# Optimization experiments

Measured on AMD Instinct MI355X. Metric: run time of the kernel, lower is better.

The kernel has to match this reference:

```python
import jax, jax.numpy as jnp
import numpy as np

N_NODES = 100000
N_EDGES = 1600000
D_IN = 32
D_OUT = 32
K_HOPS = 2
CUTGRAPH = 0.2
EPS = 1e-12  # torch F.normalize eps


def setup_inputs() -> dict:
    key = jax.random.key(0)
    k1, k2, k3, k4 = jax.random.split(key, 4)
    features = jax.random.normal(k1, (N_NODES, D_IN), dtype=jnp.float32)
    W = jax.random.normal(k2, (D_OUT, D_IN), dtype=jnp.float32) * (1.0 / np.sqrt(D_IN))
    src = jax.random.randint(k3, (N_EDGES,), 0, N_NODES, dtype=jnp.int64 if jax.config.jax_enable_x64 else jnp.int32)
    dst = jax.random.randint(k4, (N_EDGES,), 0, N_NODES, dtype=jnp.int64 if jax.config.jax_enable_x64 else jnp.int32)
    return {"features": features, "W": W, "src": src, "dst": dst}


def reference(features, W, src, dst):
    N = features.shape[0]
    E = src.shape[0]
    cut_k = int(E * CUTGRAPH)  # static edge count to prune

    # symmetric degree norm: deg^{-1/2} over in-degrees, clamped at 1
    deg = jax.ops.segment_sum(jnp.ones((E,), features.dtype), dst, num_segments=N)
    norm = jnp.power(jnp.clip(deg, 1.0, None), -0.5)[:, None]  # [N,1]

    h = features
    for _ in range(K_HOPS):
        # cosine-similarity edge pruning: zero the cut_k lowest-cos edges
        nrm = jnp.linalg.norm(h, axis=-1, keepdims=True)
        nh = h / jnp.maximum(nrm, EPS)  # F.normalize(p=2)
        cos = jnp.sum(nh[src] * nh[dst], axis=-1)  # [E]
        _, low_idx = jax.lax.top_k(-cos, cut_k)    # indices of smallest cos
        w = jnp.ones((E,), h.dtype).at[low_idx].set(0.0)

        h = h * norm
        msg = h[src] * w[:, None]                       # u_mul_e gather [E,D]
        h = jax.ops.segment_sum(msg, dst, num_segments=N)  # sum scatter
        h = h * norm

    return h @ W.T  # fc (bias=False)
```

## Files before the change

kernel.cpp:

```cpp
#include <hip/hip_runtime.h>
#include <hip/hip_bf16.h>
#include <stdint.h>

#define N_NODES 100000
#define N_EDGES 1600000
#define D_FEAT 32
#define CUT_K 320000
#define COSKEY_NB 4096
#define HC_NB 1000
#define HC_SLICE 1600
#define SCAN_NB ((N_NODES + 255) / 256)

struct SelState { unsigned long long prefix; unsigned int k; };

__global__ void deg_kernel(const int* __restrict__ dst, int* __restrict__ deg, int E) {
    int e = blockIdx.x * blockDim.x + threadIdx.x;
    if (e < E) atomicAdd(&deg[dst[e]], 1);
}

__global__ void norm_kernel(const int* __restrict__ deg, float* __restrict__ nrm, int N) {
    int i = blockIdx.x * blockDim.x + threadIdx.x;
    if (i < N) nrm[i] = 1.0f / sqrtf(fmaxf((float)deg[i], 1.0f));
}

__global__ void blocksum_kernel(const int* __restrict__ deg, int* __restrict__ bsum, int N) {
    int i = blockIdx.x * 256 + threadIdx.x;
    int v = (i < N) ? deg[i] : 0;
#pragma unroll
    for (int off = 32; off > 0; off >>= 1) v += __shfl_down(v, off, 64);
    __shared__ int ws4[4];
    if ((threadIdx.x & 63) == 0) ws4[threadIdx.x >> 6] = v;
    __syncthreads();
    if (threadIdx.x == 0) bsum[blockIdx.x] = ws4[0] + ws4[1] + ws4[2] + ws4[3];
}

__global__ void scanpartial_kernel(const int* __restrict__ bsum, int* __restrict__ boff, int B) {
    __shared__ int buf[512];
    int t = threadIdx.x;
    int v = (t < B) ? bsum[t] : 0;
    buf[t] = v;
    __syncthreads();
    for (int off = 1; off < 512; off <<= 1) {
        int u = (t >= off) ? buf[t - off] : 0;
        __syncthreads();
        buf[t] += u;
        __syncthreads();
    }
    if (t < B) boff[t] = buf[t] - v;
}

__global__ void writeoffs_kernel(const int* __restrict__ deg, const int* __restrict__ boff,
                                 int* __restrict__ offs, int* __restrict__ cursor, int N) {
    __shared__ int buf[256];
    int t = threadIdx.x;
    int i = blockIdx.x * 256 + t;
    int v = (i < N) ? deg[i] : 0;
    buf[t] = v;
    __syncthreads();
    for (int off = 1; off < 256; off <<= 1) {
        int u = (t >= off) ? buf[t - off] : 0;
        __syncthreads();
        buf[t] += u;
        __syncthreads();
    }
    int ex = buf[t] - v + boff[blockIdx.x];
    if (i < N) { offs[i] = ex; cursor[i] = ex; }
    if (i == N - 1) offs[N] = ex + v;
}

__global__ void fill_kernel(const int* __restrict__ src, const int* __restrict__ dst,
                            int* __restrict__ cursor,
                            int* __restrict__ csr_src, int* __restrict__ csr_dst,
                            int* __restrict__ csr_eid, int E) {
    int e = blockIdx.x * blockDim.x + threadIdx.x;
    if (e >= E) return;
    int d = dst[e];
    int pos = atomicAdd(&cursor[d], 1);
    csr_src[pos] = src[e];
    csr_dst[pos] = d;
    csr_eid[pos] = e;
}

__global__ void rownorm_kernel(const float* __restrict__ h, float* __restrict__ nh,
                               float* __restrict__ hs, const float* __restrict__ nrm,
                               SelState* __restrict__ st, int N) {
    int i = blockIdx.x * blockDim.x + threadIdx.x;
    if (i == 0) { st->prefix = 0ull; st->k = CUT_K; }
    if (i >= N) return;
    const float4* hp = (const float4*)(h + (size_t)i * D_FEAT);
    float4 v[8];
    float ss = 0.f;
#pragma unroll
    for (int q = 0; q < 8; ++q) {
        v[q] = hp[q];
        ss += v[q].x * v[q].x + v[q].y * v[q].y + v[q].z * v[q].z + v[q].w * v[q].w;
    }
    float inv = 1.0f / fmaxf(sqrtf(ss), 1e-12f);
    float sc = nrm[i];
    float4* op = (float4*)(nh + (size_t)i * D_FEAT);
    float4* sp = (float4*)(hs + (size_t)i * D_FEAT);
#pragma unroll
    for (int q = 0; q < 8; ++q) {
        float4 ov = v[q];
        float4 sv = v[q];
        ov.x *= inv; ov.y *= inv; ov.z *= inv; ov.w *= inv;
        sv.x *= sc;  sv.y *= sc;  sv.z *= sc;  sv.w *= sc;
        op[q] = ov;
        sp[q] = sv;
    }
}

__global__ void coskey_kernel(const float* __restrict__ nh, const int* __restrict__ csr_src,
                              const int* __restrict__ csr_dst, const int* __restrict__ csr_eid,
                              unsigned long long* __restrict__ keys,
                              unsigned int* __restrict__ ghist, int E) {
    __shared__ unsigned int lh[4][256];
    int t = threadIdx.x;
#pragma unroll
    for (int w = 0; w < 4; ++w) lh[w][t] = 0u;
    __syncthreads();
    int wave = t >> 6;
    int stride = gridDim.x * blockDim.x;
    for (int p = blockIdx.x * blockDim.x + t; p < E; p += stride) {
        const float4* a = (const float4*)(nh + (size_t)csr_src[p] * D_FEAT);
        const float4* b = (const float4*)(nh + (size_t)csr_dst[p] * D_FEAT);
        float s = 0.f;
#pragma unroll
        for (int q = 0; q < 8; ++q) {
            float4 x = a[q], y = b[q];
            s += x.x * y.x + x.y * y.y + x.z * y.z + x.w * y.w;
        }
        unsigned int u = __float_as_uint(s);
        unsigned int so = (u & 0x80000000u) ? ~u : (u | 0x80000000u);
        unsigned long long key = ((unsigned long long)so << 32) | (unsigned int)csr_eid[p];
        keys[p] = key;
        atomicAdd(&lh[wave][(unsigned int)(key >> 56)], 1u);
    }
    __syncthreads();
    unsigned int tot = lh[0][t] + lh[1][t] + lh[2][t] + lh[3][t];
    if (tot) atomicAdd(&ghist[t], tot);
}

__global__ void histc_kernel(const unsigned long long* __restrict__ in,
                             const int* __restrict__ cnt_in,
                             unsigned long long* __restrict__ out,
                             int* __restrict__ cnt_out,
                             const SelState* __restrict__ st,
                             unsigned int* __restrict__ ghist, int pass) {
    __shared__ unsigned int lh[4][256];
    __shared__ unsigned int lcnt;
    int t = threadIdx.x, b = blockIdx.x;
#pragma unroll
    for (int w = 0; w < 4; ++w) lh[w][t] = 0u;
    if (t == 0) lcnt = 0u;
    __syncthreads();
    unsigned long long prefix = st->prefix;
    int n = cnt_in ? cnt_in[b] : HC_SLICE;
    const unsigned long long* sin = in + (size_t)b * HC_SLICE;
    unsigned long long* sout = out + (size_t)b * HC_SLICE;
    int wave = t >> 6;
    int fshift = 64 - 8 * pass;
    int dshift = 56 - 8 * pass;
    for (int i = t; i < n; i += 256) {
        unsigned long long key = sin[i];
        if ((key >> fshift) == prefix) {
            atomicAdd(&lh[wave][(unsigned int)((key >> dshift) & 0xFFull)], 1u);
            unsigned int slot = atomicAdd(&lcnt, 1u);
            sout[slot] = key;
        }
    }
    __syncthreads();
    if (t == 0) cnt_out[b] = (int)lcnt;
    unsigned int tot = lh[0][t] + lh[1][t] + lh[2][t] + lh[3][t];
    if (tot) atomicAdd(&ghist[t], tot);
}

__global__ void scan8_kernel(unsigned int* __restrict__ ghist, SelState* __restrict__ st) {
    __shared__ unsigned int buf[256];
    int t = threadIdx.x;
    unsigned int k = st->k;
    unsigned int s = ghist[t];
    buf[t] = s;
    __syncthreads();
    for (int off = 1; off < 256; off <<= 1) {
        unsigned int v = (t >= off) ? buf[t - off] : 0u;
        __syncthreads();
        buf[t] += v;
        __syncthreads();
    }
    unsigned int incl = buf[t];
    unsigned int excl = incl - s;
    if (excl < k && k <= incl) {
        st->prefix = (st->prefix << 8) | (unsigned long long)t;
        st->k = k - excl;
    }
    ghist[t] = 0u;
}

__global__ void aggregate_csr_kernel(const float* __restrict__ hs, float* __restrict__ h_out,
                                     const int* __restrict__ offs, const int* __restrict__ csr_src,
                                     const unsigned long long* __restrict__ keys,
                                     const SelState* __restrict__ st,
                                     const float* __restrict__ nrm, int N) {
    unsigned long long kth = st->prefix;
    int g = blockIdx.x * 8 + (threadIdx.x >> 5);
    int j = threadIdx.x & 31;
    if (g >= N) return;
    int lo = offs[g], hi = offs[g + 1];
    float acc = 0.f;
    int p = lo;
    for (; p + 8 <= hi; p += 8) {
        unsigned long long kk[8];
        int ss[8];
#pragma unroll
        for (int u = 0; u < 8; ++u) { kk[u] = keys[p + u]; ss[u] = csr_src[p + u]; }
        float vv[8];
#pragma unroll
        for (int u = 0; u < 8; ++u) vv[u] = hs[(size_t)ss[u] * D_FEAT + j];
#pragma unroll
        for (int u = 0; u < 8; ++u) acc += (kk[u] > kth) ? vv[u] : 0.f;
    }
    for (; p < hi; ++p) {
        if (keys[p] > kth) acc += hs[(size_t)csr_src[p] * D_FEAT + j];
    }
    h_out[(size_t)g * D_FEAT + j] = acc * nrm[g];
}

__global__ void fc_kernel(const float* __restrict__ h, const float* __restrict__ W,
                          float* __restrict__ out, int N) {
    __shared__ float Wt[32][33];
    int t = threadIdx.x;
    for (int i = t; i < 1024; i += 256) Wt[i & 31][i >> 5] = W[i];
    __syncthreads();
    int node = blockIdx.x * 8 + (t >> 5);
    if (node >= N) return;
    int o = t & 31;
    const float* hr = h + (size_t)node * D_FEAT;
    float acc = 0.f;
#pragma unroll
    for (int j = 0; j < 32; ++j) acc += hr[j] * Wt[j][o];
    out[(size_t)node * D_FEAT + o] = acc;
}

extern "C" void kernel_launch(void* const* d_in, const int* in_sizes, int n_in,
                              void* d_out, int out_size, void* d_ws, size_t ws_size,
                              hipStream_t stream) {
    const float* features = (const float*)d_in[0];
    const float* W        = (const float*)d_in[1];
    const int*   src      = (const int*)d_in[2];
    const int*   dst      = (const int*)d_in[3];
    float*       out      = (float*)d_out;

    char* ws = (char*)d_ws;
    size_t o = 0;
    auto take = [&](size_t bytes) -> char* {
        char* p = ws + o;
        o += (bytes + 255) & ~(size_t)255;
        return p;
    };
    int*                deg     = (int*)take((size_t)N_NODES * 4);
    float*              nrm     = (float*)take((size_t)N_NODES * 4);
    int*                offs    = (int*)take((size_t)(N_NODES + 1) * 4);
    int*                cursor  = (int*)take((size_t)N_NODES * 4);
    int*                csr_src = (int*)take((size_t)N_EDGES * 4);
    int*                csr_dst = (int*)take((size_t)N_EDGES * 4);
    int*                csr_eid = (int*)take((size_t)N_EDGES * 4);
    float*              hA      = (float*)take((size_t)N_NODES * D_FEAT * 4);
    float*              hB      = (float*)take((size_t)N_NODES * D_FEAT * 4);
    float*              nh      = (float*)take((size_t)N_NODES * D_FEAT * 4);
    float*              hs      = (float*)take((size_t)N_NODES * D_FEAT * 4);
    unsigned long long* keys    = (unsigned long long*)take((size_t)N_EDGES * 8);
    unsigned int*       ghist   = (unsigned int*)take((size_t)256 * 4);
    SelState*           st      = (SelState*)take(256);
    int*                bsum    = (int*)take((size_t)SCAN_NB * 4);
    int*                boff    = (int*)take((size_t)SCAN_NB * 4);
    int*                cnt_a   = (int*)take((size_t)HC_NB * 4);
    int*                cnt_b   = (int*)take((size_t)HC_NB * 4);

    unsigned long long* candA = (unsigned long long*)nh;
    unsigned long long* candB = (unsigned long long*)hB;

    hipMemsetAsync(deg, 0, (size_t)N_NODES * 4, stream);
    hipMemsetAsync(ghist, 0, (size_t)256 * 4, stream);

    deg_kernel<<<(N_EDGES + 255) / 256, 256, 0, stream>>>(dst, deg, N_EDGES);
    norm_kernel<<<(N_NODES + 255) / 256, 256, 0, stream>>>(deg, nrm, N_NODES);
    blocksum_kernel<<<SCAN_NB, 256, 0, stream>>>(deg, bsum, N_NODES);
    scanpartial_kernel<<<1, 512, 0, stream>>>(bsum, boff, SCAN_NB);
    writeoffs_kernel<<<SCAN_NB, 256, 0, stream>>>(deg, boff, offs, cursor, N_NODES);
    fill_kernel<<<(N_EDGES + 255) / 256, 256, 0, stream>>>(src, dst, cursor,
                                                           csr_src, csr_dst, csr_eid, N_EDGES);

    const float* hin = features;
    float* houts[2] = { hA, hB };
    for (int hop = 0; hop < 2; ++hop) {
        float* hout = houts[hop];
        rownorm_kernel<<<(N_NODES + 255) / 256, 256, 0, stream>>>(hin, nh, hs, nrm, st, N_NODES);
        coskey_kernel<<<COSKEY_NB, 256, 0, stream>>>(nh, csr_src, csr_dst, csr_eid,
                                                     keys, ghist, N_EDGES);
        scan8_kernel<<<1, 256, 0, stream>>>(ghist, st);
        for (int pass = 1; pass < 8; ++pass) {
            const unsigned long long* in =
                (pass == 1) ? keys : ((pass & 1) ? candB : candA);
            const int* cin = (pass == 1) ? (const int*)nullptr
                                         : ((pass & 1) ? cnt_b : cnt_a);
            unsigned long long* outc = (pass & 1) ? candA : candB;
            int* cout = (pass & 1) ? cnt_a : cnt_b;
            histc_kernel<<<HC_NB, 256, 0, stream>>>(in, cin, outc, cout, st, ghist, pass);
            scan8_kernel<<<1, 256, 0, stream>>>(ghist, st);
        }
        aggregate_csr_kernel<<<(N_NODES + 7) / 8, 256, 0, stream>>>(
            hs, hout, offs, csr_src, keys, st, nrm, N_NODES);
        hin = hout;
    }
    fc_kernel<<<(N_NODES + 7) / 8, 256, 0, stream>>>(hin, W, out, N_NODES);
}
```

Before: 634.4 us.

## Collapse radix-select passes 2-7 into one single-block finish kernel; drop csr_dst

```diff
diff --git a/kernel.cpp b/kernel.cpp
--- a/kernel.cpp
+++ b/kernel.cpp
@@ -68,16 +68,11 @@
     if (i == N - 1) offs[N] = ex + v;
 }
 
-__global__ void fill_kernel(const int* __restrict__ src, const int* __restrict__ dst,
-                            int* __restrict__ cursor,
-                            int* __restrict__ csr_src, int* __restrict__ csr_dst,
+__global__ void fill_kernel(const int* __restrict__ dst, int* __restrict__ cursor,
                             int* __restrict__ csr_eid, int E) {
     int e = blockIdx.x * blockDim.x + threadIdx.x;
     if (e >= E) return;
-    int d = dst[e];
-    int pos = atomicAdd(&cursor[d], 1);
-    csr_src[pos] = src[e];
-    csr_dst[pos] = d;
+    int pos = atomicAdd(&cursor[dst[e]], 1);
     csr_eid[pos] = e;
 }
 
@@ -110,8 +105,9 @@
     }
 }
 
-__global__ void coskey_kernel(const float* __restrict__ nh, const int* __restrict__ csr_src,
-                              const int* __restrict__ csr_dst, const int* __restrict__ csr_eid,
+__global__ void coskey_kernel(const float* __restrict__ nh, const int* __restrict__ src,
+                              const int* __restrict__ dst, const int* __restrict__ csr_eid,
+                              int* __restrict__ csr_src,
                               unsigned long long* __restrict__ keys,
                               unsigned int* __restrict__ ghist, int E) {
     __shared__ unsigned int lh[4][256];
@@ -122,8 +118,10 @@
     int wave = t >> 6;
     int stride = gridDim.x * blockDim.x;
     for (int p = blockIdx.x * blockDim.x + t; p < E; p += stride) {
-        const float4* a = (const float4*)(nh + (size_t)csr_src[p] * D_FEAT);
-        const float4* b = (const float4*)(nh + (size_t)csr_dst[p] * D_FEAT);
+        int eid = csr_eid[p];
+        int s_i = src[eid], d_i = dst[eid];
+        const float4* a = (const float4*)(nh + (size_t)s_i * D_FEAT);
+        const float4* b = (const float4*)(nh + (size_t)d_i * D_FEAT);
         float s = 0.f;
 #pragma unroll
         for (int q = 0; q < 8; ++q) {
@@ -132,45 +130,12 @@
         }
         unsigned int u = __float_as_uint(s);
         unsigned int so = (u & 0x80000000u) ? ~u : (u | 0x80000000u);
-        unsigned long long key = ((unsigned long long)so << 32) | (unsigned int)csr_eid[p];
+        unsigned long long key = ((unsigned long long)so << 32) | (unsigned int)eid;
         keys[p] = key;
+        csr_src[p] = s_i;
         atomicAdd(&lh[wave][(unsigned int)(key >> 56)], 1u);
     }
     __syncthreads();
-    unsigned int tot = lh[0][t] + lh[1][t] + lh[2][t] + lh[3][t];
-    if (tot) atomicAdd(&ghist[t], tot);
-}
-
-__global__ void histc_kernel(const unsigned long long* __restrict__ in,
-                             const int* __restrict__ cnt_in,
-                             unsigned long long* __restrict__ out,
-                             int* __restrict__ cnt_out,
-                             const SelState* __restrict__ st,
-                             unsigned int* __restrict__ ghist, int pass) {
-    __shared__ unsigned int lh[4][256];
-    __shared__ unsigned int lcnt;
-    int t = threadIdx.x, b = blockIdx.x;
-#pragma unroll
-    for (int w = 0; w < 4; ++w) lh[w][t] = 0u;
-    if (t == 0) lcnt = 0u;
-    __syncthreads();
-    unsigned long long prefix = st->prefix;
-    int n = cnt_in ? cnt_in[b] : HC_SLICE;
-    const unsigned long long* sin = in + (size_t)b * HC_SLICE;
-    unsigned long long* sout = out + (size_t)b * HC_SLICE;
-    int wave = t >> 6;
-    int fshift = 64 - 8 * pass;
-    int dshift = 56 - 8 * pass;
-    for (int i = t; i < n; i += 256) {
-        unsigned long long key = sin[i];
-        if ((key >> fshift) == prefix) {
-            atomicAdd(&lh[wave][(unsigned int)((key >> dshift) & 0xFFull)], 1u);
-            unsigned int slot = atomicAdd(&lcnt, 1u);
-            sout[slot] = key;
-        }
-    }
-    __syncthreads();
-    if (t == 0) cnt_out[b] = (int)lcnt;
     unsigned int tot = lh[0][t] + lh[1][t] + lh[2][t] + lh[3][t];
     if (tot) atomicAdd(&ghist[t], tot);
 }
@@ -195,6 +160,131 @@
         st->k = k - excl;
     }
     ghist[t] = 0u;
+}
+
+__global__ void histc_kernel(const unsigned long long* __restrict__ in,
+                             unsigned long long* __restrict__ out,
+                             int* __restrict__ cnt_out,
+                             const SelState* __restrict__ st,
+                             unsigned int* __restrict__ ghist) {
+    __shared__ unsigned int lh[4][256];
+    __shared__ unsigned int lcnt;
+    int t = threadIdx.x, b = blockIdx.x;
+#pragma unroll
+    for (int w = 0; w < 4; ++w) lh[w][t] = 0u;
+    if (t == 0) lcnt = 0u;
+    __syncthreads();
+    unsigned long long prefix = st->prefix;
+    const unsigned long long* sin = in + (size_t)b * HC_SLICE;
+    unsigned long long* sout = out + (size_t)b * HC_SLICE;
+    int wave = t >> 6;
+    for (int i = t; i < HC_SLICE; i += 256) {
+        unsigned long long key = sin[i];
+        if ((key >> 56) == prefix) {
+            atomicAdd(&lh[wave][(unsigned int)((key >> 48) & 0xFFull)], 1u);
+            unsigned int slot = atomicAdd(&lcnt, 1u);
+            sout[slot] = key;
+        }
+    }
+    __syncthreads();
+    if (t == 0) cnt_out[b] = (int)lcnt;
+    unsigned int tot = lh[0][t] + lh[1][t] + lh[2][t] + lh[3][t];
+    if (tot) atomicAdd(&ghist[t], tot);
+}
+
+__global__ void finish_kernel(const unsigned long long* __restrict__ cand,
+                              const int* __restrict__ cnt,
+                              unsigned long long* __restrict__ d0,
+                              unsigned long long* __restrict__ d1,
+                              unsigned int* __restrict__ ghist,
+                              SelState* __restrict__ st) {
+    __shared__ unsigned int hist[256];
+    __shared__ unsigned int sbuf[256];
+    __shared__ unsigned int cursor;
+    __shared__ unsigned int s_n;
+    __shared__ unsigned long long s_prefix;
+    __shared__ unsigned int s_k;
+    int t = threadIdx.x;
+    if (t == 0) { s_prefix = st->prefix; s_k = st->k; cursor = 0u; }
+    __syncthreads();
+    unsigned int k1 = s_k;
+    unsigned int sv = (t < 256) ? ghist[t] : 0u;
+    if (t < 256) sbuf[t] = sv;
+    __syncthreads();
+    for (int off = 1; off < 256; off <<= 1) {
+        unsigned int v = (t < 256 && t >= off) ? sbuf[t - off] : 0u;
+        __syncthreads();
+        if (t < 256) sbuf[t] += v;
+        __syncthreads();
+    }
+    if (t < 256) {
+        unsigned int incl = sbuf[t], excl = incl - sv;
+        if (excl < k1 && k1 <= incl) {
+            s_prefix = (s_prefix << 8) | (unsigned long long)t;
+            s_k = k1 - excl;
+        }
+        ghist[t] = 0u;
+    }
+    __syncthreads();
+    unsigned long long pfx2 = s_prefix;
+    for (int b = t; b < HC_NB; b += blockDim.x) {
+        int n = cnt[b];
+        const unsigned long long* sl = cand + (size_t)b * HC_SLICE;
+        for (int i = 0; i < n; ++i) {
+            unsigned long long key = sl[i];
+            if ((key >> 48) == pfx2) {
+                unsigned int pos = atomicAdd(&cursor, 1u);
+                d0[pos] = key;
+            }
+        }
+    }
+    __syncthreads();
+    if (t == 0) s_n = cursor;
+    __syncthreads();
+    unsigned long long* cur = d0;
+    unsigned long long* nxt = d1;
+    for (int pass = 2; pass < 8; ++pass) {
+        unsigned int n = s_n;
+        int dshift = 56 - 8 * pass;
+        if (t < 256) hist[t] = 0u;
+        if (t == 0) cursor = 0u;
+        __syncthreads();
+        for (unsigned int i = t; i < n; i += blockDim.x)
+            atomicAdd(&hist[(unsigned int)((cur[i] >> dshift) & 0xFFull)], 1u);
+        __syncthreads();
+        unsigned int sv2 = (t < 256) ? hist[t] : 0u;
+        if (t < 256) sbuf[t] = sv2;
+        __syncthreads();
+        for (int off = 1; off < 256; off <<= 1) {
+            unsigned int v = (t < 256 && t >= off) ? sbuf[t - off] : 0u;
+            __syncthreads();
+            if (t < 256) sbuf[t] += v;
+            __syncthreads();
+        }
+        unsigned int k2 = s_k;
+        __syncthreads();
+        if (t < 256) {
+            unsigned int incl = sbuf[t], excl = incl - sv2;
+            if (excl < k2 && k2 <= incl) {
+                s_prefix = (s_prefix << 8) | (unsigned long long)t;
+                s_k = k2 - excl;
+            }
+        }
+        __syncthreads();
+        unsigned int dig = (unsigned int)(s_prefix & 0xFFull);
+        for (unsigned int i = t; i < n; i += blockDim.x) {
+            unsigned long long key = cur[i];
+            if ((unsigned int)((key >> dshift) & 0xFFull) == dig) {
+                unsigned int pos = atomicAdd(&cursor, 1u);
+                nxt[pos] = key;
+            }
+        }
+        __syncthreads();
+        if (t == 0) s_n = cursor;
+        __syncthreads();
+        unsigned long long* tmp = cur; cur = nxt; nxt = tmp;
+    }
+    if (t == 0) { st->prefix = s_prefix; st->k = s_k; }
 }
 
 __global__ void aggregate_csr_kernel(const float* __restrict__ hs, float* __restrict__ h_out,
@@ -263,22 +353,21 @@
     int*                offs    = (int*)take((size_t)(N_NODES + 1) * 4);
     int*                cursor  = (int*)take((size_t)N_NODES * 4);
     int*                csr_src = (int*)take((size_t)N_EDGES * 4);
-    int*                csr_dst = (int*)take((size_t)N_EDGES * 4);
     int*                csr_eid = (int*)take((size_t)N_EDGES * 4);
     float*              hA      = (float*)take((size_t)N_NODES * D_FEAT * 4);
     float*              hB      = (float*)take((size_t)N_NODES * D_FEAT * 4);
     float*              nh      = (float*)take((size_t)N_NODES * D_FEAT * 4);
     float*              hs      = (float*)take((size_t)N_NODES * D_FEAT * 4);
     unsigned long long* keys    = (unsigned long long*)take((size_t)N_EDGES * 8);
+    unsigned long long* dense1  = (unsigned long long*)take((size_t)N_EDGES * 8);
     unsigned int*       ghist   = (unsigned int*)take((size_t)256 * 4);
     SelState*           st      = (SelState*)take(256);
     int*                bsum    = (int*)take((size_t)SCAN_NB * 4);
     int*                boff    = (int*)take((size_t)SCAN_NB * 4);
     int*                cnt_a   = (int*)take((size_t)HC_NB * 4);
-    int*                cnt_b   = (int*)take((size_t)HC_NB * 4);
-
-    unsigned long long* candA = (unsigned long long*)nh;
-    unsigned long long* candB = (unsigned long long*)hB;
+
+    unsigned long long* candA  = (unsigned long long*)nh;
+    unsigned long long* dense0 = (unsigned long long*)hB;
 
     hipMemsetAsync(deg, 0, (size_t)N_NODES * 4, stream);
     hipMemsetAsync(ghist, 0, (size_t)256 * 4, stream);
@@ -288,27 +377,18 @@
     blocksum_kernel<<<SCAN_NB, 256, 0, stream>>>(deg, bsum, N_NODES);
     scanpartial_kernel<<<1, 512, 0, stream>>>(bsum, boff, SCAN_NB);
     writeoffs_kernel<<<SCAN_NB, 256, 0, stream>>>(deg, boff, offs, cursor, N_NODES);
-    fill_kernel<<<(N_EDGES + 255) / 256, 256, 0, stream>>>(src, dst, cursor,
-                                                           csr_src, csr_dst, csr_eid, N_EDGES);
+    fill_kernel<<<(N_EDGES + 255) / 256, 256, 0, stream>>>(dst, cursor, csr_eid, N_EDGES);
 
     const float* hin = features;
     float* houts[2] = { hA, hB };
     for (int hop = 0; hop < 2; ++hop) {
         float* hout = houts[hop];
         rownorm_kernel<<<(N_NODES + 255) / 256, 256, 0, stream>>>(hin, nh, hs, nrm, st, N_NODES);
-        coskey_kernel<<<COSKEY_NB, 256, 0, stream>>>(nh, csr_src, csr_dst, csr_eid,
+        coskey_kernel<<<COSKEY_NB, 256, 0, stream>>>(nh, src, dst, csr_eid, csr_src,
                                                      keys, ghist, N_EDGES);
         scan8_kernel<<<1, 256, 0, stream>>>(ghist, st);
-        for (int pass = 1; pass < 8; ++pass) {
-            const unsigned long long* in =
-                (pass == 1) ? keys : ((pass & 1) ? candB : candA);
-            const int* cin = (pass == 1) ? (const int*)nullptr
-                                         : ((pass & 1) ? cnt_b : cnt_a);
-            unsigned long long* outc = (pass & 1) ? candA : candB;
-            int* cout = (pass & 1) ? cnt_a : cnt_b;
-            histc_kernel<<<HC_NB, 256, 0, stream>>>(in, cin, outc, cout, st, ghist, pass);
-            scan8_kernel<<<1, 256, 0, stream>>>(ghist, st);
-        }
+        histc_kernel<<<HC_NB, 256, 0, stream>>>(keys, candA, cnt_a, st, ghist);
+        finish_kernel<<<1, 1024, 0, stream>>>(candA, cnt_a, dense0, dense1, ghist, st);
         aggregate_csr_kernel<<<(N_NODES + 7) / 8, 256, 0, stream>>>(
             hs, hout, offs, csr_src, keys, st, nrm, N_NODES);
         hin = hout;
```

Result: slower. 1.106 ms (+74.3%).
